# Kernel optimization log

Measured on AMD Instinct MI355X. Metric: run time of the kernel, lower is better.

Reference implementation:

```python
import jax, jax.numpy as jnp
import numpy as np

B, L, H, NH, HD, M, NL, V, RD, NS = 4, 512, 768, 12, 64, 3072, 6, 32000, 128, 2
EPS = 1e-12
COEF = 1.0 / float(np.sqrt(HD))
NEG_INF = float('-inf')


def _ln(x, scale, bias):
    x = x - jnp.mean(x, axis=-1, keepdims=True)
    x = x * jax.lax.rsqrt(jnp.mean(jnp.square(x), axis=-1, keepdims=True) + EPS)
    return x * scale + bias


def setup_inputs() -> dict:
    key = jax.random.key(0)
    ks = jax.random.split(key, 16)
    def p(k, shape):
        return jax.random.normal(k, shape, jnp.float32) * 0.02
    return dict(
        token_ids=jax.random.randint(ks[0], (B, L), 0, V, jnp.int32),
        segment_ids=jax.random.randint(ks[1], (B, L), 0, NS, jnp.int32),
        input_mask=jnp.ones((B, L), jnp.int32),
        tok_emb=p(ks[2], (V, H)),
        seg_emb=p(ks[3], (NS, H)),
        emb_scale=jnp.ones((H,), jnp.float32),
        emb_bias=jnp.zeros((H,), jnp.float32),
        Wq=p(ks[4], (NL, H, NH, HD)), bq=jnp.zeros((NL, NH, HD), jnp.float32),
        Wk=p(ks[5], (NL, H, NH, HD)), bk=jnp.zeros((NL, NH, HD), jnp.float32),
        Wv=p(ks[6], (NL, H, NH, HD)), bv=jnp.zeros((NL, NH, HD), jnp.float32),
        relpos=p(ks[7], (NL, 2 * RD - 1, H)),
        Wo=p(ks[8], (NL, NH, HD, H)), bo=jnp.zeros((NL, H), jnp.float32),
        ln1_s=jnp.ones((NL, H), jnp.float32), ln1_b=jnp.zeros((NL, H), jnp.float32),
        W1=p(ks[9], (NL, H, M)), b1=jnp.zeros((NL, M), jnp.float32),
        W2=p(ks[10], (NL, M, H)), b2=jnp.zeros((NL, H), jnp.float32),
        ln2_s=jnp.ones((NL, H), jnp.float32), ln2_b=jnp.zeros((NL, H), jnp.float32),
    )


def _encoder(token_ids, segment_ids, input_mask,
             tok_emb, seg_emb, emb_scale, emb_bias,
             Wq, bq, Wk, bk, Wv, bv, relpos, Wo, bo,
             ln1_s, ln1_b, W1, b1, W2, b2, ln2_s, ln2_b):
    # Embedding block: token + segment embeddings, layer norm (dropout = eval/no-op)
    x = tok_emb[token_ids] + seg_emb[segment_ids]            # [B, L, H]
    x = _ln(x, emb_scale, emb_bias)
    mask = jnp.where(input_mask.astype(bool), 0.0, NEG_INF)[:, None, None, :]  # [B,1,1,L]

    for i in range(NL):
        # --- relative-position self-attention ---
        q = jnp.einsum('bqe,ehd->bqhd', x, Wq[i]) + bq[i]
        k = jnp.einsum('bke,ehd->bkhd', x, Wk[i]) + bk[i]
        v = jnp.einsum('bke,ehd->bkhd', x, Wv[i]) + bv[i]
        att = jnp.einsum('bqhd,bkhd->bhqk', q, k) + mask      # [B,NH,L,L]
        # skew trick: embed absolute [L,L] scores into relative [L, 2L-1] layout
        att = jnp.pad(att, [(0, 0), (0, 0), (0, 0), (0, L - 2)], constant_values=NEG_INF)
        att = att.reshape(att.shape[:2] + (L * (2 * L - 2),))
        att = jnp.pad(att, [(0, 0), (0, 0), (L - 1, 1)], constant_values=NEG_INF)
        att = att.reshape(att.shape[:2] + (L, 2 * L - 1))     # [B,NH,L,2L-1]
        # relative-position key/value embeddings, edge-padded to 2L-1 rows
        pad = L - RD
        rel_emb = jnp.pad(relpos[i], [(pad, pad), (0, 0)], mode='edge')  # [2L-1, H]
        k_rel = jnp.einsum('re,ehd->rhd', rel_emb, Wk[i]) + bk[i]
        att = (att + jnp.einsum('bqhd,rhd->bhqr', q, k_rel)) * COEF
        probs = jax.nn.softmax(att, axis=-1)                  # [B,NH,L,2L-1]
        v_rel = jnp.einsum('re,ehd->rhd', rel_emb, Wv[i]) + bv[i]
        rel_ctx = jnp.einsum('bhqr,rhd->bqhd', probs, v_rel)
        # un-skew probs back to [B,NH,L,L] for the absolute-position context
        p = probs.reshape(probs.shape[:2] + (L * (2 * L - 1),))[:, :, L - 1:-1]
        p = p.reshape(probs.shape[:2] + (L, 2 * L - 2))[:, :, :, :L]
        ctx = jnp.einsum('bhqk,bkhd->bqhd', p, v) + rel_ctx
        y = jnp.einsum('bqhd,hde->bqe', ctx, Wo[i]) + bo[i]
        x = _ln(x + y, ln1_s[i], ln1_b[i])
        # --- MLP block ---
        y = jax.nn.gelu(jnp.einsum('bqe,em->bqm', x, W1[i]) + b1[i])
        y = jnp.einsum('bqm,me->bqe', y, W2[i]) + b2[i]
        x = _ln(x + y, ln2_s[i], ln2_b[i])
    return x


def reference(token_ids, segment_ids, input_mask,
              tok_emb, seg_emb, emb_scale, emb_bias,
              Wq, bq, Wk, bk, Wv, bv, relpos, Wo, bo,
              ln1_s, ln1_b, W1, b1, W2, b2, ln2_s, ln2_b):
    return _encoder(token_ids, segment_ids, input_mask,
                    tok_emb, seg_emb, emb_scale, emb_bias,
                    Wq, bq, Wk, bk, Wv, bv, relpos, Wo, bo,
                    ln1_s, ln1_b, W1, b1, W2, b2, ln2_s, ln2_b)
```

## Files before the change

### kernel.cpp

```cpp
#include <hip/hip_runtime.h>
#include <hip/hip_bf16.h>
#include <math.h>

#define B_   4
#define L_   512
#define H_   768
#define NH_  12
#define HD_  64
#define M_   3072
#define NL_  6
#define RD_  128
#define NR_  255
#define ROWS (B_*L_)
#define MEXT 2304
#define COEF_ 0.125f

typedef __attribute__((ext_vector_type(8))) short bf16x8;
typedef __attribute__((ext_vector_type(4))) float f32x4;


static __device__ __forceinline__ float wave_reduce_sum(float v) {
#pragma unroll
    for (int off = 32; off > 0; off >>= 1) v += __shfl_xor(v, off, 64);
    return v;
}

static __device__ __forceinline__ float gelu_f(float x) {
    float x3 = x * x * x;
    return 0.5f * x * (1.f + tanhf(0.7978845608028654f * (x + 0.044715f * x3)));
}

static __device__ __forceinline__ unsigned short f2bfu(float v) {
    __hip_bfloat16 h = __float2bfloat16(v);
    return *(unsigned short*)&h;
}

static __device__ __forceinline__ float bfu2f(unsigned short u) {
    union { float f; unsigned int i; } x;
    x.i = ((unsigned int)u) << 16;
    return x.f;
}

static __device__ __forceinline__ void gload16(const void* g, void* l) {
    __builtin_amdgcn_global_load_lds(
        (const __attribute__((address_space(1))) void*)g,
        (__attribute__((address_space(3))) void*)l,
        16, 0, 0);
}


__global__ __launch_bounds__(256) void embed_ln_kernel(
    const int* __restrict__ tok, const int* __restrict__ seg,
    const float* __restrict__ temb, const float* __restrict__ semb,
    const float* __restrict__ sc, const float* __restrict__ bi,
    float* __restrict__ out, __hip_bfloat16* __restrict__ outb)
{
    int row = blockIdx.x;
    int t = threadIdx.x;
    int tid = tok[row], sid = seg[row];
    const float* tp = temb + (size_t)tid * H_;
    const float* sp = semb + (size_t)sid * H_;
    float v[3];
#pragma unroll
    for (int j = 0; j < 3; j++) { int idx = t + j * 256; v[j] = tp[idx] + sp[idx]; }

    __shared__ float red[4];
    __shared__ float bc;
    int lane = t & 63, wid = t >> 6;

    float s = v[0] + v[1] + v[2];
    s = wave_reduce_sum(s);
    if (lane == 0) red[wid] = s;
    __syncthreads();
    if (t == 0) bc = (red[0] + red[1] + red[2] + red[3]) * (1.f / H_);
    __syncthreads();
    float mean = bc;

    float c[3]; float ss = 0.f;
#pragma unroll
    for (int j = 0; j < 3; j++) { c[j] = v[j] - mean; ss += c[j] * c[j]; }
    ss = wave_reduce_sum(ss);
    __syncthreads();
    if (lane == 0) red[wid] = ss;
    __syncthreads();
    if (t == 0) bc = rsqrtf((red[0] + red[1] + red[2] + red[3]) * (1.f / H_) + 1e-12f);
    __syncthreads();
    float r = bc;
#pragma unroll
    for (int j = 0; j < 3; j++) {
        int idx = t + j * 256;
        float o = c[j] * r * sc[idx] + bi[idx];
        out[(size_t)row * H_ + idx] = o;
        outb[(size_t)row * H_ + idx] = __float2bfloat16(o);
    }
}


__global__ __launch_bounds__(256) void add_ln_kernel(
    const float* __restrict__ x, const float* __restrict__ p0,
    const float* __restrict__ p1, const float* __restrict__ p2,
    const float* __restrict__ bias,
    const float* __restrict__ sc, const float* __restrict__ bi,
    float* __restrict__ out, __hip_bfloat16* __restrict__ outb)
{
    int row = blockIdx.x;
    int t = threadIdx.x;
    const float* xp = x + (size_t)row * H_;
    const float* q0 = p0 + (size_t)row * H_;
    const float* q1 = p1 ? p1 + (size_t)row * H_ : nullptr;
    const float* q2 = p2 ? p2 + (size_t)row * H_ : nullptr;
    float v[3];
#pragma unroll
    for (int j = 0; j < 3; j++) {
        int idx = t + j * 256;
        float a = xp[idx] + q0[idx];
        if (q1) a += q1[idx];
        if (q2) a += q2[idx];
        if (bias) a += bias[idx];
        v[j] = a;
    }

    __shared__ float red[4];
    __shared__ float bc;
    int lane = t & 63, wid = t >> 6;

    float s = v[0] + v[1] + v[2];
    s = wave_reduce_sum(s);
    if (lane == 0) red[wid] = s;
    __syncthreads();
    if (t == 0) bc = (red[0] + red[1] + red[2] + red[3]) * (1.f / H_);
    __syncthreads();
    float mean = bc;

    float c[3]; float ss = 0.f;
#pragma unroll
    for (int j = 0; j < 3; j++) { c[j] = v[j] - mean; ss += c[j] * c[j]; }
    ss = wave_reduce_sum(ss);
    __syncthreads();
    if (lane == 0) red[wid] = ss;
    __syncthreads();
    if (t == 0) bc = rsqrtf((red[0] + red[1] + red[2] + red[3]) * (1.f / H_) + 1e-12f);
    __syncthreads();
    float r = bc;
#pragma unroll
    for (int j = 0; j < 3; j++) {
        int idx = t + j * 256;
        float o = c[j] * r * sc[idx] + bi[idx];
        out[(size_t)row * H_ + idx] = o;
        if (outb) outb[(size_t)row * H_ + idx] = __float2bfloat16(o);
    }
}


__global__ __launch_bounds__(256) void pack_layer_kernel(
    const float* __restrict__ wq, const float* __restrict__ wk, const float* __restrict__ wv,
    const float* __restrict__ wo, const float* __restrict__ w1, const float* __restrict__ w2,
    const float* __restrict__ bqL, const float* __restrict__ bkL, const float* __restrict__ bvL,
    const float* __restrict__ relL,
    __hip_bfloat16* __restrict__ WtQ, __hip_bfloat16* __restrict__ WtO,
    __hip_bfloat16* __restrict__ WtW1, __hip_bfloat16* __restrict__ WtW2,
    float* __restrict__ qkvbias, __hip_bfloat16* __restrict__ relb)
{
    const int z = blockIdx.z;
    const int t = threadIdx.x;
    if (z == 6) {
        int id = blockIdx.y * 96 + blockIdx.x;
        if (id < 765) {
            int i = id * 256 + t;
            relb[i] = __float2bfloat16(relL[i]);
        } else if (id < 774) {
            int i = (id - 765) * 256 + t;
            if (i < 2304)
                qkvbias[i] = i < 768 ? bqL[i] : (i < 1536 ? bkL[i - 768] : bvL[i - 1536]);
        }
        return;
    }
    const float* in; __hip_bfloat16* out; int K, N;
    int bx = blockIdx.x, by = blockIdx.y;
    if (z < 4) {
        if (bx >= 24) return;
        K = 768; N = 768;
        in = (z == 0) ? wq : (z == 1) ? wk : (z == 2) ? wv : wo;
        out = (z < 3) ? WtQ + (size_t)z * H_ * H_ : WtO;
    } else if (z == 4) {
        K = 768; N = 3072; in = w1; out = WtW1;
    } else {
        K = 3072; N = 768; in = w2; out = WtW2;
        int tmp = bx; bx = by; by = tmp;
    }
    __shared__ float tile[32][33];
    int bX = bx * 32, bY = by * 32;
    int tx = t & 31, ty = t >> 5;
#pragma unroll
    for (int i = 0; i < 4; i++)
        tile[ty + 8 * i][tx] = in[(size_t)(bY + ty + 8 * i) * N + bX + tx];
    __syncthreads();
#pragma unroll
    for (int i = 0; i < 4; i++)
        out[(size_t)(bX + ty + 8 * i) * K + bY + tx] = __float2bfloat16(tile[tx][ty + 8 * i]);
}


__global__ __launch_bounds__(256) void transpose_vvr_kernel(
    const __hip_bfloat16* __restrict__ qkvb,
    __hip_bfloat16* __restrict__ vT, __hip_bfloat16* __restrict__ vrT)
{
    __shared__ unsigned short tile[64][72];
    const int bx = blockIdx.x;
    const int h  = blockIdx.y;
    const int t = threadIdx.x;
    const int r = t >> 2, c0 = (t & 3) * 16;
    if (bx < 32) {
        const int kb = bx * 64;
        const unsigned short* src = (const unsigned short*)qkvb + (size_t)(kb + r) * 2304 + 1536 + h * 64 + c0;
        *(uint4*)&tile[r][c0]     = *(const uint4*)src;
        *(uint4*)&tile[r][c0 + 8] = *(const uint4*)(src + 8);
        __syncthreads();
        unsigned short outv[16];
#pragma unroll
        for (int i = 0; i < 16; i++) outv[i] = tile[c0 + i][r];
        unsigned short* dst = (unsigned short*)vT +
            ((size_t)((kb >> 9) * NH_ + h) * 64 + r) * 512 + (kb & 511) + c0;
        *(uint4*)dst       = *(uint4*)&outv[0];
        *(uint4*)(dst + 8) = *(uint4*)&outv[8];
    } else {
        const int jb = (bx - 32) * 64;
        const int j = jb + r;
        if (j < NR_) {
            const unsigned short* src = (const unsigned short*)qkvb + (size_t)(2048 + j) * 2304 + 1536 + h * 64 + c0;
            *(uint4*)&tile[r][c0]     = *(const uint4*)src;
            *(uint4*)&tile[r][c0 + 8] = *(const uint4*)(src + 8);
        } else {
#pragma unroll
            for (int i = 0; i < 16; i++) tile[r][c0 + i] = 0;
        }
        __syncthreads();
        unsigned short outv[16];
#pragma unroll
        for (int i = 0; i < 16; i++) outv[i] = tile[c0 + i][r];
        unsigned short* dst = (unsigned short*)vrT + ((size_t)(h * 64) + r) * 256 + jb + c0;
        *(uint4*)dst       = *(uint4*)&outv[0];
        *(uint4*)(dst + 8) = *(uint4*)&outv[8];
    }
}


#define TK 64

__global__ __launch_bounds__(512, 6) void gemm_bf16_kernel(
    const __hip_bfloat16* __restrict__ A, const __hip_bfloat16* __restrict__ Bt,
    const float* __restrict__ bias, float* __restrict__ Cf, __hip_bfloat16* __restrict__ Cb,
    float* __restrict__ CfX, size_t xstride,
    int M, int N, int K, int act, int ksplit)
{
    __shared__ __hip_bfloat16 As[2][128 * TK];
    __shared__ __hip_bfloat16 Bs[2][64 * TK];
    const int t = threadIdx.x;
    const int lane = t & 63;
    const int wid = t >> 6;
    const int lq = lane & 15, lg = lane >> 4;
    const int wm = (wid & 3) * 32, wn = (wid >> 2) * 32;

    const int nbx = gridDim.x;
    const int nwg = nbx * gridDim.y;
    int wgid = blockIdx.y * nbx + blockIdx.x;
    if ((nwg & 7) == 0) { int qq = nwg >> 3; wgid = (wgid & 7) * qq + (wgid >> 3); }
    const int bm = (wgid / nbx) * 128, bn = (wgid % nbx) * 64;
    const int kbase = blockIdx.z * ksplit;

    f32x4 acc[2][2];
#pragma unroll
    for (int i = 0; i < 2; i++)
#pragma unroll
        for (int j = 0; j < 2; j++) acc[i][j] = (f32x4){0.f, 0.f, 0.f, 0.f};

    const int rl = t >> 3;
    const int cswz = (((t & 7) * 16) ^ ((rl & 7) << 4)) >> 1;
    const __hip_bfloat16* ga[2];
    const __hip_bfloat16* gb;
    int lofsA[2], lofsB;
#pragma unroll
    for (int c = 0; c < 2; c++) {
        int rowa = bm + c * 64 + rl; if (rowa >= M) rowa = M - 1;
        ga[c] = A + (size_t)rowa * K + kbase + cswz;
        lofsA[c] = (c * 64 + wid * 8) * TK;
    }
    gb = Bt + (size_t)(bn + rl) * K + kbase + cswz;
    lofsB = (wid * 8) * TK;

    const int nt = ksplit / TK;
    gload16(ga[0], &As[0][lofsA[0]]);
    gload16(ga[1], &As[0][lofsA[1]]);
    gload16(gb,    &Bs[0][lofsB]);
    __syncthreads();

    int cur = 0;
    for (int kt = 0; kt < nt; kt++) {
        if (kt + 1 < nt) {
            const int koff = (kt + 1) * TK;
            gload16(ga[0] + koff, &As[cur ^ 1][lofsA[0]]);
            gload16(ga[1] + koff, &As[cur ^ 1][lofsA[1]]);
            gload16(gb + koff,    &Bs[cur ^ 1][lofsB]);
        }
#pragma unroll
        for (int kh = 0; kh < 2; kh++) {
            const int kb = kh * 64 + lg * 16;
            bf16x8 af[2], bfr[2];
#pragma unroll
            for (int i = 0; i < 2; i++) {
                int ra = wm + i * 16 + lq;
                af[i] = *(const bf16x8*)((const char*)&As[cur][0] + ra * 128 + (kb ^ ((ra & 7) << 4)));
            }
#pragma unroll
            for (int j = 0; j < 2; j++) {
                int rb = wn + j * 16 + lq;
                bfr[j] = *(const bf16x8*)((const char*)&Bs[cur][0] + rb * 128 + (kb ^ ((rb & 7) << 4)));
            }
#pragma unroll
            for (int i = 0; i < 2; i++)
#pragma unroll
                for (int j = 0; j < 2; j++)
                    acc[i][j] = __builtin_amdgcn_mfma_f32_16x16x32_bf16(af[i], bfr[j], acc[i][j], 0, 0, 0);
        }
        __syncthreads();
        cur ^= 1;
    }

    float* outf = (blockIdx.z == 0) ? Cf : (CfX + (size_t)(blockIdx.z - 1) * xstride);
#pragma unroll
    for (int i = 0; i < 2; i++) {
#pragma unroll
        for (int j = 0; j < 2; j++) {
            int col = bn + wn + j * 16 + lq;
            float bsv = bias ? bias[col] : 0.f;
            int row0 = bm + wm + i * 16 + lg * 4;
#pragma unroll
            for (int rr = 0; rr < 4; rr++) {
                int row = row0 + rr;
                if (row >= M) continue;
                float v = acc[i][j][rr] + bsv;
                if (act) v = gelu_f(v);
                if (Cb && blockIdx.z == 0) Cb[(size_t)row * N + col] = __float2bfloat16(v);
                else                       outf[(size_t)row * N + col] = v;
            }
        }
    }
}


#define PS_LD 520
#define PR_LD 264

__global__ __launch_bounds__(256, 3) void attn_kernel(
    const __hip_bfloat16* __restrict__ qkvb,
    const __hip_bfloat16* __restrict__ vT,
    const __hip_bfloat16* __restrict__ vrT,
    const int* __restrict__ mask,
    __hip_bfloat16* __restrict__ ctxb)
{
    __shared__ unsigned short RqPrel[32 * PR_LD];
    __shared__ unsigned short Ps[32 * PS_LD];
    __shared__ float mstat[32 * 4];
    __shared__ float sstat[32 * 4];
    __shared__ float maskb[512];

    const int i_ = blockIdx.x;
    const int c_ = i_ & 7, s_ = i_ >> 3;
    const int p_ = c_ + 8 * (s_ >> 4);
    const int qt = s_ & 15;
    const int b = p_ / 12, h = p_ % 12;

    const int t = threadIdx.x;
    const int lane = t & 63, w = t >> 6;
    const int lq = lane & 15, lg = lane >> 4;

    maskb[t]       = mask[b * L_ + t]       ? 0.f : -1e30f;
    maskb[t + 256] = mask[b * L_ + t + 256] ? 0.f : -1e30f;

    const char* Qbase  = (const char*)qkvb + ((size_t)(b * L_ + qt * 32) * 2304 + h * 64) * 2;
    const char* Kbase  = (const char*)qkvb + ((size_t)(b * L_) * 2304 + 768 + h * 64) * 2;
    const char* KRbase = (const char*)qkvb + ((size_t)2048 * 2304 + 768 + h * 64) * 2;

    bf16x8 afq[2][2];
#pragma unroll
    for (int ks = 0; ks < 2; ks++) {
        const int kofs = ks * 64 + lg * 16;
        afq[ks][0] = *(const bf16x8*)(Qbase + (size_t)lq * 4608 + kofs);
        afq[ks][1] = *(const bf16x8*)(Qbase + (size_t)(16 + lq) * 4608 + kofs);
    }

    {
        f32x4 accr[2][4];
#pragma unroll
        for (int i = 0; i < 2; i++)
#pragma unroll
            for (int j = 0; j < 4; j++) accr[i][j] = (f32x4){0.f, 0.f, 0.f, 0.f};
#pragma unroll
        for (int ks = 0; ks < 2; ks++) {
            const int kofs = ks * 64 + lg * 16;
            bf16x8 bkr_[4];
#pragma unroll
            for (int jt = 0; jt < 4; jt++) {
                int j = w * 64 + jt * 16 + lq;
                int jr = j > 254 ? 254 : j;
                bkr_[jt] = *(const bf16x8*)(KRbase + (size_t)jr * 4608 + kofs);
            }
#pragma unroll
            for (int jt = 0; jt < 4; jt++) {
                accr[0][jt] = __builtin_amdgcn_mfma_f32_16x16x32_bf16(afq[ks][0], bkr_[jt], accr[0][jt], 0, 0, 0);
                accr[1][jt] = __builtin_amdgcn_mfma_f32_16x16x32_bf16(afq[ks][1], bkr_[jt], accr[1][jt], 0, 0, 0);
            }
        }
#pragma unroll
        for (int it = 0; it < 2; it++)
#pragma unroll
            for (int jt = 0; jt < 4; jt++)
#pragma unroll
                for (int r = 0; r < 4; r++)
                    RqPrel[(it * 16 + lg * 4 + r) * PR_LD + w * 64 + jt * 16 + lq] = f2bfu(accr[it][jt][r]);
    }
    __syncthreads();

    f32x4 accs[2][8];
#pragma unroll
    for (int i = 0; i < 2; i++)
#pragma unroll
        for (int j = 0; j < 8; j++) accs[i][j] = (f32x4){0.f, 0.f, 0.f, 0.f};
#pragma unroll
    for (int ks = 0; ks < 2; ks++) {
        const int kofs = ks * 64 + lg * 16;
        bf16x8 bk_[8];
#pragma unroll
        for (int jt = 0; jt < 8; jt++) {
            int key = w * 128 + jt * 16 + lq;
            bk_[jt] = *(const bf16x8*)(Kbase + (size_t)key * 4608 + kofs);
        }
#pragma unroll
        for (int jt = 0; jt < 8; jt++) {
            accs[0][jt] = __builtin_amdgcn_mfma_f32_16x16x32_bf16(afq[ks][0], bk_[jt], accs[0][jt], 0, 0, 0);
            accs[1][jt] = __builtin_amdgcn_mfma_f32_16x16x32_bf16(afq[ks][1], bk_[jt], accs[1][jt], 0, 0, 0);
        }
    }

#pragma unroll
    for (int it = 0; it < 2; it++) {
#pragma unroll
        for (int r = 0; r < 4; r++) {
            int q = it * 16 + lg * 4 + r;
            int qg = qt * 32 + q;
            float mx = -INFINITY;
#pragma unroll
            for (int jt = 0; jt < 8; jt++) {
                int k = w * 128 + jt * 16 + lq;
                int jc = k - qg + 127;
                jc = jc < 0 ? 0 : (jc > 254 ? 254 : jc);
                float s = (accs[it][jt][r] + bfu2f(RqPrel[q * PR_LD + jc])) * COEF_ + maskb[k];
                accs[it][jt][r] = s;
                mx = fmaxf(mx, s);
            }
#pragma unroll
            for (int off = 1; off < 16; off <<= 1) mx = fmaxf(mx, __shfl_xor(mx, off, 64));
            if (lq == 0) mstat[q * 4 + w] = mx;
        }
    }
    __syncthreads();

#pragma unroll
    for (int it = 0; it < 2; it++) {
#pragma unroll
        for (int r = 0; r < 4; r++) {
            int q = it * 16 + lg * 4 + r;
            float4 mv = *(const float4*)&mstat[q * 4];
            float gm = fmaxf(fmaxf(mv.x, mv.y), fmaxf(mv.z, mv.w));
            float ssum = 0.f;
#pragma unroll
            for (int jt = 0; jt < 8; jt++) {
                int k = w * 128 + jt * 16 + lq;
                float p = __expf(accs[it][jt][r] - gm);
                ssum += p;
                Ps[q * PS_LD + k] = f2bfu(p);
            }
#pragma unroll
            for (int off = 1; off < 16; off <<= 1) ssum += __shfl_xor(ssum, off, 64);
            if (lq == 0) sstat[q * 4 + w] = ssum;
        }
    }
    __syncthreads();

    const __hip_bfloat16* vTb  = vT  + (((size_t)(b * NH_ + h) * 64) + w * 16 + lq) * 512 + lg * 8;
    const __hip_bfloat16* vrTb = vrT + ((size_t)(h * 64) + w * 16 + lq) * 256 + lg * 8;
    bf16x8 bvpre[8], vrpre[8];
#pragma unroll
    for (int ks = 0; ks < 8; ks++) {
        bvpre[ks] = *(const bf16x8*)(vTb + ks * 32);
        vrpre[ks] = *(const bf16x8*)(vrTb + ks * 32);
    }
    {
        int q = t >> 3, sub = t & 7;
        int qg = qt * 32 + q;
#pragma unroll
        for (int jj = 0; jj < 32; jj++) {
            int j = sub + 8 * jj;
            if (j == 0 || j == 254) continue;
            if (j == 255) { RqPrel[q * PR_LD + 255] = 0; continue; }
            int k = qg + j - 127;
            unsigned short val = ((unsigned)k < 512u) ? Ps[q * PS_LD + k] : (unsigned short)0;
            RqPrel[q * PR_LD + j] = val;
        }
    }
    {
        int task = t >> 2, ts = t & 3;
        int q = task >> 1, side = task & 1;
        int qg = qt * 32 + q;
        float sum = 0.f;
        if (side == 0) {
            int hi = qg - 127;
            for (int k = ts; k <= hi; k += 4) sum += bfu2f(Ps[q * PS_LD + k]);
        } else {
            for (int k = qg + 127 + ts; k < 512; k += 4) sum += bfu2f(Ps[q * PS_LD + k]);
        }
        sum += __shfl_xor(sum, 1, 64);
        sum += __shfl_xor(sum, 2, 64);
        if (ts == 0) RqPrel[q * PR_LD + (side == 0 ? 0 : 254)] = f2bfu(sum);
    }
    __syncthreads();

    f32x4 accv[2];
    accv[0] = (f32x4){0.f, 0.f, 0.f, 0.f};
    accv[1] = (f32x4){0.f, 0.f, 0.f, 0.f};

#pragma unroll
    for (int ks = 0; ks < 8; ks++) {
        bf16x8 pa0 = *(const bf16x8*)((const char*)Ps + (size_t)lq * (PS_LD * 2) + ks * 64 + lg * 16);
        bf16x8 pa1 = *(const bf16x8*)((const char*)Ps + (size_t)(16 + lq) * (PS_LD * 2) + ks * 64 + lg * 16);
        accv[0] = __builtin_amdgcn_mfma_f32_16x16x32_bf16(pa0, bvpre[ks], accv[0], 0, 0, 0);
        accv[1] = __builtin_amdgcn_mfma_f32_16x16x32_bf16(pa1, bvpre[ks], accv[1], 0, 0, 0);
    }
#pragma unroll
    for (int ks = 8; ks < 16; ks++) {
        bf16x8 bv = *(const bf16x8*)(vTb + ks * 32);
        bf16x8 pa0 = *(const bf16x8*)((const char*)Ps + (size_t)lq * (PS_LD * 2) + ks * 64 + lg * 16);
        bf16x8 pa1 = *(const bf16x8*)((const char*)Ps + (size_t)(16 + lq) * (PS_LD * 2) + ks * 64 + lg * 16);
        accv[0] = __builtin_amdgcn_mfma_f32_16x16x32_bf16(pa0, bv, accv[0], 0, 0, 0);
        accv[1] = __builtin_amdgcn_mfma_f32_16x16x32_bf16(pa1, bv, accv[1], 0, 0, 0);
    }
#pragma unroll
    for (int ks = 0; ks < 8; ks++) {
        bf16x8 pa0 = *(const bf16x8*)((const char*)RqPrel + (size_t)lq * (PR_LD * 2) + ks * 64 + lg * 16);
        bf16x8 pa1 = *(const bf16x8*)((const char*)RqPrel + (size_t)(16 + lq) * (PR_LD * 2) + ks * 64 + lg * 16);
        accv[0] = __builtin_amdgcn_mfma_f32_16x16x32_bf16(pa0, vrpre[ks], accv[0], 0, 0, 0);
        accv[1] = __builtin_amdgcn_mfma_f32_16x16x32_bf16(pa1, vrpre[ks], accv[1], 0, 0, 0);
    }

#pragma unroll
    for (int it = 0; it < 2; it++) {
#pragma unroll
        for (int r = 0; r < 4; r++) {
            int q = it * 16 + lg * 4 + r;
            float4 sv = *(const float4*)&sstat[q * 4];
            float inv = 1.f / (sv.x + sv.y + sv.z + sv.w);
            ctxb[(size_t)(b * L_ + qt * 32 + q) * 768 + h * 64 + w * 16 + lq] =
                __float2bfloat16(accv[it][r] * inv);
        }
    }
}


extern "C" void kernel_launch(void* const* d_in, const int* in_sizes, int n_in,
                              void* d_out, int out_size, void* d_ws, size_t ws_size,
                              hipStream_t stream)
{
    const int*   tok    = (const int*)d_in[0];
    const int*   seg    = (const int*)d_in[1];
    const int*   maskp  = (const int*)d_in[2];
    const float* temb   = (const float*)d_in[3];
    const float* semb   = (const float*)d_in[4];
    const float* esc    = (const float*)d_in[5];
    const float* ebi    = (const float*)d_in[6];
    const float* Wq     = (const float*)d_in[7];
    const float* bq     = (const float*)d_in[8];
    const float* Wk     = (const float*)d_in[9];
    const float* bk     = (const float*)d_in[10];
    const float* Wv     = (const float*)d_in[11];
    const float* bv     = (const float*)d_in[12];
    const float* relpos = (const float*)d_in[13];
    const float* Wo     = (const float*)d_in[14];
    const float* bo     = (const float*)d_in[15];
    const float* ln1s   = (const float*)d_in[16];
    const float* ln1b   = (const float*)d_in[17];
    const float* W1     = (const float*)d_in[18];
    const float* b1     = (const float*)d_in[19];
    const float* W2     = (const float*)d_in[20];
    const float* b2     = (const float*)d_in[21];
    const float* ln2s   = (const float*)d_in[22];
    const float* ln2b   = (const float*)d_in[23];

    const size_t NX = (size_t)ROWS * H_;
    float* x       = (float*)d_ws;
    float* x2      = x + NX;
    float* y       = x2 + NX;
    float* qkvbias = y + NX;
    __hip_bfloat16* xb    = (__hip_bfloat16*)(qkvbias + 2304);
    __hip_bfloat16* x2b   = xb    + (size_t)MEXT * H_;
    __hip_bfloat16* ctxb  = x2b   + NX;
    __hip_bfloat16* qkvb  = ctxb  + NX;
    __hip_bfloat16* vT    = qkvb  + (size_t)MEXT * 2304;
    __hip_bfloat16* vrT   = vT    + (size_t)B_ * NH_ * 64 * 512;
    __hip_bfloat16* WtQ   = vrT   + (size_t)NH_ * 64 * 256;
    __hip_bfloat16* WtO   = WtQ   + (size_t)2304 * H_;
    __hip_bfloat16* WtW1  = WtO   + (size_t)H_ * H_;
    __hip_bfloat16* WtW2  = WtW1  + (size_t)M_ * H_;
    __hip_bfloat16* h1b   = WtW2  + (size_t)H_ * M_;

    float* spill = (float*)qkvb;

    dim3 blk(256);
    dim3 blk512(512);

    embed_ln_kernel<<<ROWS, blk, 0, stream>>>(tok, seg, temb, semb, esc, ebi, x, xb);

    for (int l = 0; l < NL_; l++) {
        const float* wq = Wq + (size_t)l * H_ * H_;
        const float* wk = Wk + (size_t)l * H_ * H_;
        const float* wv = Wv + (size_t)l * H_ * H_;
        const float* wo = Wo + (size_t)l * H_ * H_;
        const float* w1 = W1 + (size_t)l * H_ * M_;
        const float* w2 = W2 + (size_t)l * M_ * H_;

        pack_layer_kernel<<<dim3(96, 24, 7), blk, 0, stream>>>(
            wq, wk, wv, wo, w1, w2,
            bq + (size_t)l * H_, bk + (size_t)l * H_, bv + (size_t)l * H_,
            relpos + (size_t)l * NR_ * H_,
            WtQ, WtO, WtW1, WtW2, qkvbias, xb + (size_t)ROWS * H_);

        gemm_bf16_kernel<<<dim3(36, 18), blk512, 0, stream>>>(xb, WtQ, qkvbias, nullptr, qkvb, nullptr, 0,
                                                              MEXT, 2304, H_, 0, H_);
        transpose_vvr_kernel<<<dim3(36, 12), blk, 0, stream>>>(qkvb, vT, vrT);

        attn_kernel<<<dim3(768), blk, 0, stream>>>(qkvb, vT, vrT, maskp, ctxb);

        gemm_bf16_kernel<<<dim3(12, 16, 2), blk512, 0, stream>>>(ctxb, WtO, nullptr, y, nullptr, spill, NX,
                                                                 ROWS, H_, H_, 0, 384);
        add_ln_kernel<<<ROWS, blk, 0, stream>>>(x, y, spill, nullptr, bo + (size_t)l * H_,
                                                ln1s + (size_t)l * H_, ln1b + (size_t)l * H_, x2, x2b);

        gemm_bf16_kernel<<<dim3(48, 16), blk512, 0, stream>>>(x2b, WtW1, b1 + (size_t)l * M_, nullptr, h1b, nullptr, 0,
                                                              ROWS, M_, H_, 1, H_);
        gemm_bf16_kernel<<<dim3(12, 16, 3), blk512, 0, stream>>>(h1b, WtW2, nullptr, y, nullptr, spill, NX,
                                                                 ROWS, H_, M_, 0, 1024);

        float* outp = (l == NL_ - 1) ? (float*)d_out : x;
        __hip_bfloat16* outbp = (l == NL_ - 1) ? nullptr : xb;
        add_ln_kernel<<<ROWS, blk, 0, stream>>>(x2, y, spill, spill + NX, b2 + (size_t)l * H_,
                                                ln2s + (size_t)l * H_, ln2b + (size_t)l * H_, outp, outbp);
    }
}
```

Baseline: 732.0 us.

## Split GEMM A-source for relpos rows, fine-grained waitcnt barriers, prefetch in attention

The GEMM kernel gains a second A pointer, so relative-position embedding rows come from a separate buffer instead of being appended after the activations. Its K loop replaces __syncthreads with explicit vmcnt waits plus raw s_barrier, letting the next tile's global loads stay in flight during compute. The attention kernel issues K loads for both k-slices up front, moves the relpos score store after those loads, drops one barrier, and prefetches the V-rel fragments earlier. The aim is to hide memory latency, at the cost of more registers and reliance on hand-placed wait counts being correct.

After: 737.6 us. About the same (+0.8%).

```diff
diff --git a/kernel.cpp b/kernel.cpp
--- a/kernel.cpp
+++ b/kernel.cpp
@@ -248,7 +248,8 @@
 #define TK 64
 
 __global__ __launch_bounds__(512, 6) void gemm_bf16_kernel(
-    const __hip_bfloat16* __restrict__ A, const __hip_bfloat16* __restrict__ Bt,
+    const __hip_bfloat16* __restrict__ A, const __hip_bfloat16* __restrict__ A2,
+    const __hip_bfloat16* __restrict__ Bt,
     const float* __restrict__ bias, float* __restrict__ Cf, __hip_bfloat16* __restrict__ Cb,
     float* __restrict__ CfX, size_t xstride,
     int M, int N, int K, int act, int ksplit)
@@ -281,8 +282,16 @@
     int lofsA[2], lofsB;
 #pragma unroll
     for (int c = 0; c < 2; c++) {
-        int rowa = bm + c * 64 + rl; if (rowa >= M) rowa = M - 1;
-        ga[c] = A + (size_t)rowa * K + kbase + cswz;
+        int rowa = bm + c * 64 + rl;
+        const __hip_bfloat16* base;
+        if (A2 && rowa >= ROWS) {
+            int rr = rowa - ROWS; if (rr > NR_ - 1) rr = NR_ - 1;
+            base = A2 + (size_t)rr * K;
+        } else {
+            if (rowa >= M) rowa = M - 1;
+            base = A + (size_t)rowa * K;
+        }
+        ga[c] = base + kbase + cswz;
         lofsA[c] = (c * 64 + wid * 8) * TK;
     }
     gb = Bt + (size_t)(bn + rl) * K + kbase + cswz;
@@ -292,7 +301,6 @@
     gload16(ga[0], &As[0][lofsA[0]]);
     gload16(ga[1], &As[0][lofsA[1]]);
     gload16(gb,    &Bs[0][lofsB]);
-    __syncthreads();
 
     int cur = 0;
     for (int kt = 0; kt < nt; kt++) {
@@ -301,7 +309,12 @@
             gload16(ga[0] + koff, &As[cur ^ 1][lofsA[0]]);
             gload16(ga[1] + koff, &As[cur ^ 1][lofsA[1]]);
             gload16(gb + koff,    &Bs[cur ^ 1][lofsB]);
-        }
+            asm volatile("s_waitcnt vmcnt(3)" ::: "memory");
+        } else {
+            asm volatile("s_waitcnt vmcnt(0)" ::: "memory");
+        }
+        __builtin_amdgcn_sched_barrier(0);
+        __builtin_amdgcn_s_barrier();
 #pragma unroll
         for (int kh = 0; kh < 2; kh++) {
             const int kb = kh * 64 + lg * 16;
@@ -322,7 +335,7 @@
                 for (int j = 0; j < 2; j++)
                     acc[i][j] = __builtin_amdgcn_mfma_f32_16x16x32_bf16(af[i], bfr[j], acc[i][j], 0, 0, 0);
         }
-        __syncthreads();
+        __builtin_amdgcn_s_barrier();
         cur ^= 1;
     }
 
@@ -389,58 +402,68 @@
         afq[ks][1] = *(const bf16x8*)(Qbase + (size_t)(16 + lq) * 4608 + kofs);
     }
 
-    {
-        f32x4 accr[2][4];
-#pragma unroll
-        for (int i = 0; i < 2; i++)
-#pragma unroll
-            for (int j = 0; j < 4; j++) accr[i][j] = (f32x4){0.f, 0.f, 0.f, 0.f};
-#pragma unroll
-        for (int ks = 0; ks < 2; ks++) {
-            const int kofs = ks * 64 + lg * 16;
-            bf16x8 bkr_[4];
-#pragma unroll
-            for (int jt = 0; jt < 4; jt++) {
-                int j = w * 64 + jt * 16 + lq;
-                int jr = j > 254 ? 254 : j;
-                bkr_[jt] = *(const bf16x8*)(KRbase + (size_t)jr * 4608 + kofs);
-            }
-#pragma unroll
-            for (int jt = 0; jt < 4; jt++) {
-                accr[0][jt] = __builtin_amdgcn_mfma_f32_16x16x32_bf16(afq[ks][0], bkr_[jt], accr[0][jt], 0, 0, 0);
-                accr[1][jt] = __builtin_amdgcn_mfma_f32_16x16x32_bf16(afq[ks][1], bkr_[jt], accr[1][jt], 0, 0, 0);
-            }
-        }
-#pragma unroll
-        for (int it = 0; it < 2; it++)
-#pragma unroll
-            for (int jt = 0; jt < 4; jt++)
-#pragma unroll
-                for (int r = 0; r < 4; r++)
-                    RqPrel[(it * 16 + lg * 4 + r) * PR_LD + w * 64 + jt * 16 + lq] = f2bfu(accr[it][jt][r]);
-    }
-    __syncthreads();
-
-    f32x4 accs[2][8];
+    f32x4 accr[2][4];
 #pragma unroll
     for (int i = 0; i < 2; i++)
 #pragma unroll
-        for (int j = 0; j < 8; j++) accs[i][j] = (f32x4){0.f, 0.f, 0.f, 0.f};
+        for (int j = 0; j < 4; j++) accr[i][j] = (f32x4){0.f, 0.f, 0.f, 0.f};
 #pragma unroll
     for (int ks = 0; ks < 2; ks++) {
         const int kofs = ks * 64 + lg * 16;
-        bf16x8 bk_[8];
-#pragma unroll
-        for (int jt = 0; jt < 8; jt++) {
-            int key = w * 128 + jt * 16 + lq;
-            bk_[jt] = *(const bf16x8*)(Kbase + (size_t)key * 4608 + kofs);
-        }
-#pragma unroll
-        for (int jt = 0; jt < 8; jt++) {
-            accs[0][jt] = __builtin_amdgcn_mfma_f32_16x16x32_bf16(afq[ks][0], bk_[jt], accs[0][jt], 0, 0, 0);
-            accs[1][jt] = __builtin_amdgcn_mfma_f32_16x16x32_bf16(afq[ks][1], bk_[jt], accs[1][jt], 0, 0, 0);
-        }
-    }
+        bf16x8 bkr_[4];
+#pragma unroll
+        for (int jt = 0; jt < 4; jt++) {
+            int j = w * 64 + jt * 16 + lq;
+            int jr = j > 254 ? 254 : j;
+            bkr_[jt] = *(const bf16x8*)(KRbase + (size_t)jr * 4608 + kofs);
+        }
+#pragma unroll
+        for (int jt = 0; jt < 4; jt++) {
+            accr[0][jt] = __builtin_amdgcn_mfma_f32_16x16x32_bf16(afq[ks][0], bkr_[jt], accr[0][jt], 0, 0, 0);
+            accr[1][jt] = __builtin_amdgcn_mfma_f32_16x16x32_bf16(afq[ks][1], bkr_[jt], accr[1][jt], 0, 0, 0);
+        }
+    }
+
+    bf16x8 bk0_[8], bk1_[8];
+#pragma unroll
+    for (int jt = 0; jt < 8; jt++) {
+        int key = w * 128 + jt * 16 + lq;
+        bk0_[jt] = *(const bf16x8*)(Kbase + (size_t)key * 4608 + lg * 16);
+        bk1_[jt] = *(const bf16x8*)(Kbase + (size_t)key * 4608 + 64 + lg * 16);
+    }
+
+#pragma unroll
+    for (int it = 0; it < 2; it++)
+#pragma unroll
+        for (int jt = 0; jt < 4; jt++)
+#pragma unroll
+            for (int r = 0; r < 4; r++)
+                RqPrel[(it * 16 + lg * 4 + r) * PR_LD + w * 64 + jt * 16 + lq] = f2bfu(accr[it][jt][r]);
+
+    f32x4 accs[2][8];
+#pragma unroll
+    for (int i = 0; i < 2; i++)
+#pragma unroll
+        for (int j = 0; j < 8; j++) accs[i][j] = (f32x4){0.f, 0.f, 0.f, 0.f};
+#pragma unroll
+    for (int jt = 0; jt < 8; jt++) {
+        accs[0][jt] = __builtin_amdgcn_mfma_f32_16x16x32_bf16(afq[0][0], bk0_[jt], accs[0][jt], 0, 0, 0);
+        accs[1][jt] = __builtin_amdgcn_mfma_f32_16x16x32_bf16(afq[0][1], bk0_[jt], accs[1][jt], 0, 0, 0);
+    }
+#pragma unroll
+    for (int jt = 0; jt < 8; jt++) {
+        accs[0][jt] = __builtin_amdgcn_mfma_f32_16x16x32_bf16(afq[1][0], bk1_[jt], accs[0][jt], 0, 0, 0);
+        accs[1][jt] = __builtin_amdgcn_mfma_f32_16x16x32_bf16(afq[1][1], bk1_[jt], accs[1][jt], 0, 0, 0);
+    }
+
+    const __hip_bfloat16* vTb  = vT  + (((size_t)(b * NH_ + h) * 64) + w * 16 + lq) * 512 + lg * 8;
+    const __hip_bfloat16* vrTb = vrT + ((size_t)(h * 64) + w * 16 + lq) * 256 + lg * 8;
+    bf16x8 vrpre[8];
+#pragma unroll
+    for (int ks = 0; ks < 8; ks++)
+        vrpre[ks] = *(const bf16x8*)(vrTb + ks * 32);
+
+    __syncthreads();
 
 #pragma unroll
     for (int it = 0; it < 2; it++) {
@@ -487,14 +510,10 @@
     }
     __syncthreads();
 
-    const __hip_bfloat16* vTb  = vT  + (((size_t)(b * NH_ + h) * 64) + w * 16 + lq) * 512 + lg * 8;
-    const __hip_bfloat16* vrTb = vrT + ((size_t)(h * 64) + w * 16 + lq) * 256 + lg * 8;
-    bf16x8 bvpre[8], vrpre[8];
-#pragma unroll
-    for (int ks = 0; ks < 8; ks++) {
+    bf16x8 bvpre[8];
+#pragma unroll
+    for (int ks = 0; ks < 8; ks++)
         bvpre[ks] = *(const bf16x8*)(vTb + ks * 32);
-        vrpre[ks] = *(const bf16x8*)(vrTb + ks * 32);
-    }
     {
         int q = t >> 3, sub = t & 7;
         int qg = qt * 32 + q;
@@ -601,12 +620,13 @@
     float* y       = x2 + NX;
     float* qkvbias = y + NX;
     __hip_bfloat16* xb    = (__hip_bfloat16*)(qkvbias + 2304);
-    __hip_bfloat16* x2b   = xb    + (size_t)MEXT * H_;
+    __hip_bfloat16* x2b   = xb    + NX;
     __hip_bfloat16* ctxb  = x2b   + NX;
     __hip_bfloat16* qkvb  = ctxb  + NX;
     __hip_bfloat16* vT    = qkvb  + (size_t)MEXT * 2304;
     __hip_bfloat16* vrT   = vT    + (size_t)B_ * NH_ * 64 * 512;
-    __hip_bfloat16* WtQ   = vrT   + (size_t)NH_ * 64 * 256;
+    __hip_bfloat16* relb  = vrT   + (size_t)NH_ * 64 * 256;
+    __hip_bfloat16* WtQ   = relb  + (size_t)NR_ * H_;
     __hip_bfloat16* WtO   = WtQ   + (size_t)2304 * H_;
     __hip_bfloat16* WtW1  = WtO   + (size_t)H_ * H_;
     __hip_bfloat16* WtW2  = WtW1  + (size_t)M_ * H_;
@@ -631,22 +651,26 @@
             wq, wk, wv, wo, w1, w2,
             bq + (size_t)l * H_, bk + (size_t)l * H_, bv + (size_t)l * H_,
             relpos + (size_t)l * NR_ * H_,
-            WtQ, WtO, WtW1, WtW2, qkvbias, xb + (size_t)ROWS * H_);
-
-        gemm_bf16_kernel<<<dim3(36, 18), blk512, 0, stream>>>(xb, WtQ, qkvbias, nullptr, qkvb, nullptr, 0,
+            WtQ, WtO, WtW1, WtW2, qkvbias, relb);
+
+        gemm_bf16_kernel<<<dim3(36, 18), blk512, 0, stream>>>(xb, relb, WtQ, qkvbias,
+                                                              nullptr, qkvb, nullptr, 0,
                                                               MEXT, 2304, H_, 0, H_);
         transpose_vvr_kernel<<<dim3(36, 12), blk, 0, stream>>>(qkvb, vT, vrT);
 
         attn_kernel<<<dim3(768), blk, 0, stream>>>(qkvb, vT, vrT, maskp, ctxb);
 
-        gemm_bf16_kernel<<<dim3(12, 16, 2), blk512, 0, stream>>>(ctxb, WtO, nullptr, y, nullptr, spill, NX,
+        gemm_bf16_kernel<<<dim3(12, 16, 2), blk512, 0, stream>>>(ctxb, nullptr, WtO, nullptr,
+                                                                 y, nullptr, spill, NX,
                                                                  ROWS, H_, H_, 0, 384);
         add_ln_kernel<<<ROWS, blk, 0, stream>>>(x, y, spill, nullptr, bo + (size_t)l * H_,
                                                 ln1s + (size_t)l * H_, ln1b + (size_t)l * H_, x2, x2b);
 
-        gemm_bf16_kernel<<<dim3(48, 16), blk512, 0, stream>>>(x2b, WtW1, b1 + (size_t)l * M_, nullptr, h1b, nullptr, 0,
+        gemm_bf16_kernel<<<dim3(48, 16), blk512, 0, stream>>>(x2b, nullptr, WtW1, b1 + (size_t)l * M_,
+                                                              nullptr, h1b, nullptr, 0,
                                                               ROWS, M_, H_, 1, H_);
-        gemm_bf16_kernel<<<dim3(12, 16, 3), blk512, 0, stream>>>(h1b, WtW2, nullptr, y, nullptr, spill, NX,
+        gemm_bf16_kernel<<<dim3(12, 16, 3), blk512, 0, stream>>>(h1b, nullptr, WtW2, nullptr,
+                                                                 y, nullptr, spill, NX,
                                                                  ROWS, H_, M_, 0, 1024);
 
         float* outp = (l == NL_ - 1) ? (float*)d_out : x;
```
